# Kernel tuning notes

Hardware: AMD Instinct MI355X
Metric: run time of the kernel (lower is better)

## Reference

```python
import jax, jax.numpy as jnp
import numpy as np

B, H, W, D, C, K, ITERS = 16, 64, 64, 64, 16, 5, 4
EPS_LN = 1e-5

def _ln(x, g, b):
    m = x.mean(-1, keepdims=True)
    v = jnp.mean((x - m) ** 2, axis=-1, keepdims=True)
    return (x - m) / jnp.sqrt(v + EPS_LN) * g + b

def _build_grid(h, w):
    # (h, w, 2) with x in [-1,1] over width, y in [-1,1] over height
    y, x = jnp.meshgrid(jnp.linspace(-1.0, 1.0, h), jnp.linspace(-1.0, 1.0, w), indexing='ij')
    return jnp.stack([x, y], axis=-1)

def _forward(feat, feat_color, mask, slot_noise, slots_mu, slots_logsigma,
             w_grid, b_grid, w_k, w_v, ln_kv_g, ln_kv_b, w_mlp, b_mlp,
             ln_q_g, ln_q_b, w_q, w_ih, w_hh, b_ih, b_hh,
             ln_feat_g, ln_feat_b, ln_color_g, ln_color_b,
             ln_res_g, ln_res_b, w_res, b_res):
    b, h, w, d = feat.shape
    n = h * w
    k_slots = mask.shape[0]
    scale = d ** (-0.5)

    grid = _build_grid(h, w)  # (H, W, 2)

    # fg position: weighted mean of grid under mask -> (K, 2), broadcast to (B, K, 2)
    gm = grid.transpose(2, 0, 1)[None] * mask            # (K, 2, H, W)
    fg_pos = gm.sum((2, 3)) / (mask.sum((2, 3)) + 1e-5)  # (K, 2)
    fg_pos = jnp.broadcast_to(fg_pos[None], (b, k_slots, 2))

    feat_n = _ln(feat.reshape(b, n, d), ln_feat_g, ln_feat_b)                    # (B, N, D)
    featc_n = _ln(feat_color.reshape(b, n, feat_color.shape[-1]), ln_color_g, ln_color_b)

    slot = slots_mu + jnp.exp(slots_logsigma) * slot_noise  # (B, K, D)

    # k/v with relative positional grid embedding (fg_pos is constant across iters,
    # so k/v are iteration-invariant and computed once -- same math as the original loop)
    rel = grid[None, None] - fg_pos[:, :, None, None, :]        # (B, K, H, W, 2)
    rel4 = jnp.concatenate([rel, -rel], -1).reshape(b, k_slots, n, 4)
    grid_embed = rel4 @ w_grid.T + b_grid                       # (B, K, N, D)
    k = _ln(feat_n @ w_k.T[None] [0][None][0][None][0] if False else (feat_n @ w_k.T)[:, None] + grid_embed, ln_kv_g, ln_kv_b) @ w_mlp.T + b_mlp
    v = _ln((feat_n @ w_v.T)[:, None] + grid_embed, ln_kv_g, ln_kv_b) @ w_mlp.T + b_mlp

    attn = None
    for it in range(ITERS):
        prev = slot
        q = _ln(slot, ln_q_g, ln_q_b) @ w_q.T                         # (B, K, D)
        logits = jnp.einsum('bkd,bknd->bkn', q, k) * scale
        attn = jax.nn.softmax(logits, axis=-1)                        # (B, K, N)
        upd = jnp.einsum('bkn,bknd->bkd', attn, v)                    # (B, K, D)
        if it != ITERS - 1:
            # torch GRUCell
            x = upd.reshape(-1, d)
            hp = slot.reshape(-1, d)
            gi = x @ w_ih.T + b_ih
            gh = hp @ w_hh.T + b_hh
            i_r, i_z, i_n = jnp.split(gi, 3, axis=-1)
            h_r, h_z, h_n = jnp.split(gh, 3, axis=-1)
            r = jax.nn.sigmoid(i_r + h_r)
            z = jax.nn.sigmoid(i_z + h_z)
            nn_ = jnp.tanh(i_n + r * h_n)
            slot = ((1.0 - z) * nn_ + z * hp).reshape(b, k_slots, d)
            slot = _ln(slot, ln_res_g, ln_res_b) @ w_res.T + b_res + prev
        else:
            slot_color = jnp.einsum('bkn,bnc->bkc', attn, featc_n)
            slot = jnp.concatenate([slot, slot_color], axis=-1)       # (B, K, D+C)

    amin = attn.min(axis=2, keepdims=True)
    amax = attn.max(axis=2, keepdims=True)
    attn = (attn - amin) / (amax - amin + 1e-5)
    return slot, fg_pos, attn

def setup_inputs() -> dict:
    key = jax.random.key(0)
    ks = jax.random.split(key, 16)
    def rn(i, shape, s=0.02):
        return jax.random.normal(ks[i], shape, jnp.float32) * s
    return {
        'feat': jax.random.normal(ks[0], (B, H, W, D), jnp.float32),
        'feat_color': jax.random.normal(ks[1], (B, H, W, C), jnp.float32),
        'mask': jax.random.uniform(ks[2], (K, 1, H, W), jnp.float32),
        'slot_noise': jax.random.normal(ks[3], (B, K, D), jnp.float32),
        'slots_mu': rn(4, (1, 1, D), 1.0),
        'slots_logsigma': rn(5, (1, 1, D), 0.01),
        'w_grid': rn(6, (D, 4)), 'b_grid': jnp.zeros((D,), jnp.float32),
        'w_k': rn(7, (D, D)), 'w_v': rn(8, (D, D)),
        'ln_kv_g': jnp.ones((D,), jnp.float32), 'ln_kv_b': jnp.zeros((D,), jnp.float32),
        'w_mlp': rn(9, (D, D)), 'b_mlp': jnp.zeros((D,), jnp.float32),
        'ln_q_g': jnp.ones((D,), jnp.float32), 'ln_q_b': jnp.zeros((D,), jnp.float32),
        'w_q': rn(10, (D, D)),
        'w_ih': rn(11, (3 * D, D)), 'w_hh': rn(12, (3 * D, D)),
        'b_ih': jnp.zeros((3 * D,), jnp.float32), 'b_hh': jnp.zeros((3 * D,), jnp.float32),
        'ln_feat_g': jnp.ones((D,), jnp.float32), 'ln_feat_b': jnp.zeros((D,), jnp.float32),
        'ln_color_g': jnp.ones((C,), jnp.float32), 'ln_color_b': jnp.zeros((C,), jnp.float32),
        'ln_res_g': jnp.ones((D,), jnp.float32), 'ln_res_b': jnp.zeros((D,), jnp.float32),
        'w_res': rn(13, (D, D)), 'b_res': jnp.zeros((D,), jnp.float32),
    }

def reference(feat, feat_color, mask, slot_noise, slots_mu, slots_logsigma,
              w_grid, b_grid, w_k, w_v, ln_kv_g, ln_kv_b, w_mlp, b_mlp,
              ln_q_g, ln_q_b, w_q, w_ih, w_hh, b_ih, b_hh,
              ln_feat_g, ln_feat_b, ln_color_g, ln_color_b,
              ln_res_g, ln_res_b, w_res, b_res):
    return _forward(feat, feat_color, mask, slot_noise, slots_mu, slots_logsigma,
                    w_grid, b_grid, w_k, w_v, ln_kv_g, ln_kv_b, w_mlp, b_mlp,
                    ln_q_g, ln_q_b, w_q, w_ih, w_hh, b_ih, b_hh,
                    ln_feat_g, ln_feat_b, ln_color_g, ln_color_b,
                    ln_res_g, ln_res_b, w_res, b_res)
```

## Files before the change

### kernel.cpp

```cpp
#include <hip/hip_runtime.h>
#include <stdint.h>

#define B_ 16
#define H_ 64
#define W_ 64
#define D_ 64
#define C_ 16
#define K_ 5
#define N_ 4096
#define NC_ 32
#define CS_ 128
#define EPS 1e-5f

typedef __attribute__((ext_vector_type(8))) short bf16x8;
typedef __attribute__((ext_vector_type(4))) float f32x4;

__device__ __forceinline__ float wsum64(float v){
  #pragma unroll
  for(int o=1;o<64;o<<=1) v += __shfl_xor(v,o,64);
  return v;
}
__device__ __forceinline__ float wmax64(float v){
  #pragma unroll
  for(int o=1;o<64;o<<=1) v = fmaxf(v, __shfl_xor(v,o,64));
  return v;
}
__device__ __forceinline__ float wmin64(float v){
  #pragma unroll
  for(int o=1;o<64;o<<=1) v = fminf(v, __shfl_xor(v,o,64));
  return v;
}
__device__ __forceinline__ uint16_t f2bf(float f){
  uint32_t u = __float_as_uint(f);
  u += 0x7fffu + ((u>>16)&1u);
  return (uint16_t)(u>>16);
}

__global__ __launch_bounds__(256) void k_pre(
    const float* __restrict__ mask, const float* __restrict__ noise,
    const float* __restrict__ mu, const float* __restrict__ lsg,
    const float* __restrict__ wm, const float* __restrict__ bm, const float* __restrict__ lnkb,
    const float* __restrict__ wk, const float* __restrict__ wv, const float* __restrict__ lnfb,
    const float* __restrict__ wq, const float* __restrict__ lnqg, const float* __restrict__ lnqb,
    const float* __restrict__ wres, const float* __restrict__ bres,
    const float* __restrict__ lnrg, const float* __restrict__ lnrb,
    const float* __restrict__ wih, const float* __restrict__ whh,
    const float* __restrict__ wg, const float* __restrict__ bg,
    const float* __restrict__ lnfg, const float* __restrict__ lnkg,
    float* __restrict__ ws_fg, float* __restrict__ out_fg,
    float* __restrict__ bm2, float* __restrict__ fkb, float* __restrict__ fvb,
    float* __restrict__ qb, float* __restrict__ br2,
    float* __restrict__ wgx, float* __restrict__ wgy, float* __restrict__ gscal,
    float* __restrict__ wrpT,
    float* __restrict__ gw, float* __restrict__ slot, float* __restrict__ out_slot,
    float* __restrict__ WQp, float* __restrict__ WCp, float* __restrict__ bq2p,
    float* __restrict__ uvp, float* __restrict__ vqp, float* __restrict__ cscp){
  __shared__ __align__(16) float M0[64][68];
  __shared__ __align__(16) float M1[64][68];
  __shared__ __align__(16) float M2T[64][68];
  __shared__ float vtmp[4][64];
  __shared__ float aux[4][64];
  int bid=blockIdx.x, tid=threadIdx.x;

  #define MM44(SRCA, SRCB) { \
    float a4[4], b4[4]; \
    *(float4*)a4 = *(const float4*)(SRCA); \
    *(float4*)b4 = *(const float4*)(SRCB); \
    _Pragma("unroll") \
    for(int ii=0;ii<4;ii++){ \
      _Pragma("unroll") \
      for(int jj=0;jj<4;jj++) acc[ii][jj]=fmaf(a4[ii],b4[jj],acc[ii][jj]); \
    } }

  if(bid<5){
    int k=bid;
    float sm=0.f, sx=0.f, sy=0.f;
    for(int p=tid; p<H_*W_; p+=256){
      int i=p>>6, j=p&63;
      float m = mask[k*H_*W_ + p];
      float x = -1.f + (2.f/63.f)*j;
      float y = -1.f + (2.f/63.f)*i;
      sm+=m; sx+=m*x; sy+=m*y;
    }
    __shared__ float r0[4], r1[4], r2[4];
    int wid=tid>>6, lane=tid&63;
    sm=wsum64(sm); sx=wsum64(sx); sy=wsum64(sy);
    if(lane==0){ r0[wid]=sm; r1[wid]=sx; r2[wid]=sy; }
    __syncthreads();
    if(tid==0){
      float tm=r0[0]+r0[1]+r0[2]+r0[3];
      float tx=r1[0]+r1[1]+r1[2]+r1[3];
      float ty=r2[0]+r2[1]+r2[2]+r2[3];
      float px = tx/(tm+1e-5f), py = ty/(tm+1e-5f);
      ws_fg[k*2+0]=px; ws_fg[k*2+1]=py;
      for(int b=0;b<B_;b++){ out_fg[(b*K_+k)*2+0]=px; out_fg[(b*K_+k)*2+1]=py; }
    }
  } else if(bid==5){
    int sel=tid>>6, o=tid&63; float s=0.f;
    if(sel==0){ s=bm[o]; for(int d=0;d<64;d++) s+=lnkb[d]*wm[o*64+d]; bm2[o]=s; }
    else if(sel==1){ for(int d=0;d<64;d++) s+=lnqb[d]*wq[o*64+d]; qb[o]=0.125f*s; }
    else if(sel==2){ for(int d=0;d<64;d++) s+=lnrb[d]*wres[o*64+d]; br2[o]=s+bres[o]; }
    else { for(int d=0;d<64;d++) s+=lnfb[d]*wk[o*64+d]; fkb[o]=s; }
  } else if(bid==6){
    int wv4=tid>>6, l=tid&63;
    if(wv4==0){ float s=0.f; for(int d=0;d<64;d++) s+=lnfb[d]*wv[l*64+d]; fvb[l]=s; }
    else if(wv4==1){
      float4 w4 = *(const float4*)(wg + l*4);
      wgx[l]=w4.x-w4.z; wgy[l]=w4.y-w4.w;
    } else if(wv4==2){
      float4 w4 = *(const float4*)(wg + l*4);
      float wx=w4.x-w4.z, wy=w4.y-w4.w, bl=bg[l];
      float t;
      t=wsum64(wx);    if(l==0) gscal[0]=t*(1.f/64.f);
      t=wsum64(wy);    if(l==0) gscal[1]=t*(1.f/64.f);
      t=wsum64(bl);    if(l==0) gscal[2]=t*(1.f/64.f);
      t=wsum64(wx*wx); if(l==0) gscal[3]=t*(1.f/64.f);
      t=wsum64(wy*wy); if(l==0) gscal[4]=t*(1.f/64.f);
      t=wsum64(wx*wy); if(l==0) gscal[5]=t*(2.f/64.f);
      t=wsum64(wx*bl); if(l==0) gscal[6]=t*(2.f/64.f);
      t=wsum64(wy*bl); if(l==0) gscal[7]=t*(2.f/64.f);
      t=wsum64(bl*bl); if(l==0) gscal[8]=t*(1.f/64.f);
    } else {
      for(int j=l;j<B_*K_*16;j+=64){ int bk2=j>>4, cc2=j&15; out_slot[bk2*80+64+cc2]=0.f; }
    }
  } else if(bid<23){
    int i=(bid-7)*256+tid;
    int d=i>>6, o=i&63;
    wrpT[i]=lnrg[d]*wres[o*64+d];
  } else if(bid<119){
    int i=(bid-23)*256+tid;
    int g6=i>>12, r=i&4095, d=r>>6, o=r&63;
    float v = (g6<3)? wih[(g6*64+o)*64+d] : whh[((g6-3)*64+o)*64+d];
    gw[g6*4096 + d*64 + o] = v;
  } else if(bid<139){
    int i=(bid-119)*256+tid;
    if(i<B_*K_*D_){ int d=i&63; slot[i]=mu[d]+expf(lsg[d])*noise[i]; }
  } else if(bid==139){
    for(int i=tid;i<4096;i+=256){ int r=i>>6,c2=i&63; M0[r][c2]=wq[i]; M1[r][c2]=wm[i]; }
    if(tid>=192){ int l=tid-192;
      float4 w4 = *(const float4*)(wg + l*4);
      aux[0][l]=w4.x-w4.z; aux[1][l]=w4.y-w4.w; aux[2][l]=bg[l]; aux[3][l]=lnkg[l];
    }
    __syncthreads();
    if(tid<64){ float s=0.f; for(int d=0;d<64;d++) s+=lnqb[d]*M0[tid][d]; vtmp[0][tid]=0.125f*s; }
    else if(tid<128){ int c2=tid-64; float s=bm[c2]; for(int d=0;d<64;d++) s+=lnkb[d]*M1[c2][d]; vtmp[1][c2]=s; }
    else if(tid<192){ int o=tid-128; float s=0.f; for(int d=0;d<64;d++) s+=lnfb[d]*wk[o*64+d]; vtmp[2][o]=s; }
    __syncthreads();
    {
      int d0=(tid>>4)*4, e0=(tid&15)*4;
      float acc[4][4]={};
      for(int c2=0;c2<64;c2++) MM44(&M0[c2][d0], &M1[c2][e0]);
      float lq4[4]; *(float4*)lq4 = *(const float4*)(lnqg+d0);
      #pragma unroll
      for(int jj=0;jj<4;jj++){
        float w4[4];
        #pragma unroll
        for(int ii=0;ii<4;ii++) w4[ii]=0.125f*lq4[ii]*acc[ii][jj];
        *(float4*)&M2T[e0+jj][d0] = *(float4*)w4;
      }
    }
    __syncthreads();
    if(tid<64){
      int e=tid; float s=0.f; for(int c2=0;c2<64;c2++) s=fmaf(vtmp[0][c2], M1[c2][e], s); vtmp[3][e]=s;
    } else if(tid<128){
      int d=tid-64; float s=0.f; for(int c2=0;c2<64;c2++) s=fmaf(M0[c2][d], vtmp[1][c2], s);
      vqp[4*64+d]=0.125f*lnqg[d]*s;
    }
    __syncthreads();
    for(int i=tid;i<4096;i+=256){ int e=i>>6,o=i&63; M0[e][o]=aux[3][e]*wk[i]; }
    __syncthreads();
    {
      int d0=(tid>>4)*4, o0=(tid&15)*4;
      float acc[4][4]={};
      for(int e=0;e<64;e++) MM44(&M2T[e][d0], &M0[e][o0]);
      float lf4[4]; *(float4*)lf4 = *(const float4*)(lnfg+o0);
      #pragma unroll
      for(int ii=0;ii<4;ii++){
        float w4[4];
        #pragma unroll
        for(int jj=0;jj<4;jj++) w4[jj]=lf4[jj]*acc[ii][jj];
        *(float4*)(WQp + (d0+ii)*64 + o0) = *(float4*)w4;
      }
    }
    if(tid<64){ int o=tid; float s=0.f;
      for(int e=0;e<64;e++) s=fmaf(vtmp[3][e], M0[e][o], s);
      bq2p[o]=lnfg[o]*s; }
    else if(tid<128){ int d=tid-64; float s1=0.f,sx=0.f,sy=0.f,s3=0.f;
      for(int e=0;e<64;e++){ float pe=M2T[e][d]*aux[3][e];
        s1+=pe; sx+=pe*aux[0][e]; sy+=pe*aux[1][e]; s3+=pe*(aux[2][e]+vtmp[2][e]); }
      vqp[0*64+d]=s1; vqp[1*64+d]=sx; vqp[2*64+d]=sy; vqp[3*64+d]=s3; }
    else if(tid<192){
      int e=tid-128;
      float qe=vtmp[3][e]*aux[3][e];
      float c0=wsum64(qe);
      float c1=wsum64(qe*aux[0][e]);
      float c2=wsum64(qe*aux[1][e]);
      float c3=wsum64(qe*(aux[2][e]+vtmp[2][e]));
      float c4=wsum64(vtmp[0][e]*vtmp[1][e]);
      if(e==0){ cscp[0]=c0; cscp[1]=c1; cscp[2]=c2; cscp[3]=c3; cscp[4]=c4; }
    }
  } else {
    for(int i=tid;i<4096;i+=256){ int r=i>>6,c2=i&63; M0[r][c2]=wv[i]*lnkg[r]; M1[c2][r]=wm[i]; }
    if(tid>=192){ int l=tid-192;
      float4 w4 = *(const float4*)(wg + l*4);
      aux[0][l]=w4.x-w4.z; aux[1][l]=w4.y-w4.w; aux[2][l]=bg[l]; aux[3][l]=lnkg[l];
    }
    __syncthreads();
    if(tid<64){ float s=0.f; const float* wr=wv+tid*64;
      for(int d=0;d<64;d++) s+=lnfb[d]*wr[d]; vtmp[0][tid]=s; }
    __syncthreads();
    {
      int d0=(tid>>4)*4, o0=(tid&15)*4;
      float acc[4][4]={};
      for(int e=0;e<64;e++) MM44(&M0[e][d0], &M1[e][o0]);
      float lf4[4]; *(float4*)lf4 = *(const float4*)(lnfg+d0);
      #pragma unroll
      for(int ii=0;ii<4;ii++){
        float w4[4];
        #pragma unroll
        for(int jj=0;jj<4;jj++) w4[jj]=lf4[ii]*acc[ii][jj];
        *(float4*)(WCp + (d0+ii)*64 + o0) = *(float4*)w4;
      }
    }
    if(tid<64){ int o=tid; float s1=0.f,s2=0.f,s3=0.f,s4=0.f;
      for(int e=0;e<64;e++){ float we=aux[3][e]*M1[e][o];
        s1+=we*(vtmp[0][e]+aux[2][e]); s2+=we*aux[0][e]; s3+=we*aux[1][e]; s4+=we; }
      uvp[0*64+o]=s1; uvp[1*64+o]=s2; uvp[2*64+o]=s3; uvp[3*64+o]=s4; }
  }
  #undef MM44
}

__global__ __launch_bounds__(256) void k_featln(const float* __restrict__ feat,
    const float* __restrict__ wk, const float* __restrict__ wv, const float* __restrict__ gf,
    const float* __restrict__ fkb, const float* __restrict__ fvb,
    const float* __restrict__ wgx, const float* __restrict__ wgy, const float* __restrict__ bg,
    const float* __restrict__ fc, const float* __restrict__ gc, const float* __restrict__ bc,
    uint16_t* __restrict__ Aout, float4* __restrict__ kstat, float4* __restrict__ vstat,
    float* __restrict__ fcn){
  int tid=threadIdx.x, wid=tid>>6, lane=tid&63;
  int q=lane>>4, c=lane&15;
  size_t row = (size_t)blockIdx.x*64 + wid*16 + c;
  const float* xp = feat + row*64;
  float x[16];
  *(float4*)&x[0]  = *(const float4*)(xp + q*8);
  *(float4*)&x[4]  = *(const float4*)(xp + q*8 + 4);
  *(float4*)&x[8]  = *(const float4*)(xp + 32 + q*8);
  *(float4*)&x[12] = *(const float4*)(xp + 36 + q*8);
  float s=0.f;
  #pragma unroll
  for(int i=0;i<16;i++) s+=x[i];
  s += __shfl_xor(s,16,64); s += __shfl_xor(s,32,64);
  float mean = s*(1.f/64.f);
  float v=0.f;
  #pragma unroll
  for(int i=0;i<16;i++){ float d=x[i]-mean; v+=d*d; }
  v += __shfl_xor(v,16,64); v += __shfl_xor(v,32,64);
  float rs = rsqrtf(v*(1.f/64.f)+EPS);
  float gl[16];
  *(float4*)&gl[0]  = *(const float4*)(gf + q*8);
  *(float4*)&gl[4]  = *(const float4*)(gf + q*8 + 4);
  *(float4*)&gl[8]  = *(const float4*)(gf + 32 + q*8);
  *(float4*)&gl[12] = *(const float4*)(gf + 36 + q*8);
  bf16x8 A0, A1;
  #pragma unroll
  for(int j=0;j<8;j++){
    A0[j] = (short)f2bf((x[j]  -mean)*rs);
    A1[j] = (short)f2bf((x[8+j]-mean)*rs);
  }
  *(bf16x8*)(Aout + row*64 + q*8) = A0;
  *(bf16x8*)(Aout + row*64 + 32 + q*8) = A1;
  float wgxl[4][4], wgyl[4][4], bgl[4][4];
  #pragma unroll
  for(int ot=0;ot<4;ot++){
    *(float4*)&wgxl[ot][0] = *(const float4*)(wgx + ot*16 + q*4);
    *(float4*)&wgyl[ot][0] = *(const float4*)(wgy + ot*16 + q*4);
    *(float4*)&bgl[ot][0]  = *(const float4*)(bg + ot*16 + q*4);
  }
  #pragma unroll
  for(int mat=0;mat<2;mat++){
    const float* w = mat? wv : wk;
    const float* fb = mat? fvb : fkb;
    float ss=0.f, s2=0.f, dx=0.f, dy=0.f, db=0.f;
    #pragma unroll
    for(int ot=0; ot<4; ot++){
      const float* wp = w + (size_t)(ot*16+c)*64 + q*8;
      bf16x8 W0, W1;
      #pragma unroll
      for(int j=0;j<8;j++){ W0[j]=(short)f2bf(wp[j]*gl[j]); W1[j]=(short)f2bf(wp[32+j]*gl[8+j]); }
      float4 bq = *(const float4*)(fb + ot*16 + q*4);
      f32x4 acc = {bq.x,bq.y,bq.z,bq.w};
      acc = __builtin_amdgcn_mfma_f32_16x16x32_bf16(W0, A0, acc, 0,0,0);
      acc = __builtin_amdgcn_mfma_f32_16x16x32_bf16(W1, A1, acc, 0,0,0);
      #pragma unroll
      for(int r=0;r<4;r++){
        float a=acc[r];
        ss+=a; s2+=a*a;
        dx = fmaf(a, wgxl[ot][r], dx);
        dy = fmaf(a, wgyl[ot][r], dy);
        db = fmaf(a, bgl[ot][r], db);
      }
    }
    ss += __shfl_xor(ss,16,64); ss += __shfl_xor(ss,32,64);
    s2 += __shfl_xor(s2,16,64); s2 += __shfl_xor(s2,32,64);
    dx += __shfl_xor(dx,16,64); dx += __shfl_xor(dx,32,64);
    dy += __shfl_xor(dy,16,64); dy += __shfl_xor(dy,32,64);
    db += __shfl_xor(db,16,64); db += __shfl_xor(db,32,64);
    if(lane<16){
      size_t row2 = (size_t)blockIdx.x*64 + wid*16 + lane;
      float4 st = { ss*(1.f/64.f), s2*(1.f/64.f)+db*(1.f/32.f), dx*(1.f/32.f), dy*(1.f/32.f) };
      (mat? vstat : kstat)[row2] = st;
    }
  }
  int r16=tid>>4, cc=tid&15;
  #pragma unroll
  for(int i=0;i<4;i++){
    size_t row2 = (size_t)blockIdx.x*64 + i*16 + r16;
    float xv = fc[row2*16+cc];
    float sc=xv;
    #pragma unroll
    for(int o=1;o<16;o<<=1) sc += __shfl_xor(sc,o,16);
    float m2 = sc*(1.f/16.f);
    float df = xv-m2;
    float v2 = df*df;
    #pragma unroll
    for(int o=1;o<16;o<<=1) v2 += __shfl_xor(v2,o,16);
    fcn[row2*16+cc] = df*rsqrtf(v2*(1.f/16.f)+EPS)*gc[cc] + bc[cc];
  }
}

template<bool GRU>
__global__ __launch_bounds__(256) void k_slotq(
    const float* __restrict__ slot_prev, float* __restrict__ slot_cur,
    const float* __restrict__ part, const float* __restrict__ pscal,
    const float* __restrict__ red_in,
    const float* __restrict__ gw,
    const float* __restrict__ bih, const float* __restrict__ bhh,
    const float* __restrict__ wrpT, const float* __restrict__ br2,
    const float* __restrict__ bm2,
    const float* __restrict__ WQ, const float* __restrict__ bq2,
    const float* __restrict__ WC, const float* __restrict__ uvec,
    const float* __restrict__ vq, const float* __restrict__ csc,
    const float* __restrict__ gscal,
    float* __restrict__ qs_out, float* __restrict__ cst_out){
  __shared__ float vv[64], vh[64];
  __shared__ float red6[4][64][6];
  __shared__ float lamb[NC_];
  __shared__ float sc4[4];
  int bk=blockIdx.x;
  int tid=threadIdx.x, wid=tid>>6, lane=tid&63;
  int o=lane, qq=wid;
  float mwgx=gscal[0], mwgy=gscal[1], mbg=gscal[2];

  #define MV(Wptr) { float p_=0.f; \
      _Pragma("unroll") \
      for(int dd=0;dd<16;dd++) p_ = fmaf(vv[qq*16+dd], (Wptr)[(qq*16+dd)*64+o], p_); \
      red6[qq][o][0]=p_; } __syncthreads();
  #define SUM0 (red6[0][lane][0]+red6[1][lane][0]+red6[2][lane][0]+red6[3][lane][0])

  float cur=0.f, hp=0.f;
  if(GRU){
    if(wid==0){
      float m_l = (lane<NC_)? red_in[((size_t)bk*NC_+lane)*4]   : -1e30f;
      float s_l = (lane<NC_)? red_in[((size_t)bk*NC_+lane)*4+1] : 0.f;
      float M = wmax64(m_l);
      float eu = (lane<NC_)? __expf(m_l-M) : 0.f;
      float S = wsum64(s_l*eu);
      float lam = eu/S;
      if(lane<NC_) lamb[lane]=lam;
      float p0 = (lane<NC_)? pscal[((size_t)bk*NC_+lane)*4+0] : 0.f;
      float p1 = (lane<NC_)? pscal[((size_t)bk*NC_+lane)*4+1] : 0.f;
      float p2 = (lane<NC_)? pscal[((size_t)bk*NC_+lane)*4+2] : 0.f;
      float p3 = (lane<NC_)? pscal[((size_t)bk*NC_+lane)*4+3] : 0.f;
      float As = wsum64(lam*p0), Ax = wsum64(lam*p1);
      float Ay = wsum64(lam*p2), Am = wsum64(lam*p3);
      if(lane==0){ sc4[0]=As; sc4[1]=Ax; sc4[2]=Ay; sc4[3]=Am; }
    }
    __syncthreads();
    {
      float p_=0.f;
      #pragma unroll
      for(int j=0;j<8;j++){
        int cc = qq*8+j;
        p_ = fmaf(lamb[cc], part[((size_t)bk*NC_+cc)*64+o], p_);
      }
      red6[qq][o][0]=p_;
    }
    __syncthreads();
    if(wid==0) vv[lane] = SUM0;
    __syncthreads();
    MV(WC);
    if(wid==0){
      float As=sc4[0],Ax=sc4[1],Ay=sc4[2],Am=sc4[3];
      float x_ = SUM0 + As*uvec[lane] + Ax*uvec[64+lane] + Ay*uvec[128+lane]
               - Am*uvec[192+lane] + bm2[lane];
      hp = slot_prev[bk*64+lane];
      vv[lane]=x_; vh[lane]=hp;
    }
    __syncthreads();
    {
      float p0=0.f,p1=0.f,p2=0.f,p3=0.f,p4=0.f,p5=0.f;
      #pragma unroll
      for(int dd=0;dd<16;dd++){
        int d = qq*16+dd;
        float xd=vv[d], hd=vh[d];
        p0 = fmaf(xd, gw[d*64+o], p0);
        p1 = fmaf(xd, gw[4096+d*64+o], p1);
        p2 = fmaf(xd, gw[8192+d*64+o], p2);
        p3 = fmaf(hd, gw[12288+d*64+o], p3);
        p4 = fmaf(hd, gw[16384+d*64+o], p4);
        p5 = fmaf(hd, gw[20480+d*64+o], p5);
      }
      red6[qq][o][0]=p0; red6[qq][o][1]=p1; red6[qq][o][2]=p2;
      red6[qq][o][3]=p3; red6[qq][o][4]=p4; red6[qq][o][5]=p5;
    }
    __syncthreads();
    if(wid==0){
      float gir=bih[lane], giz=bih[64+lane], gin=bih[128+lane];
      float ghr=bhh[lane], ghz=bhh[64+lane], ghn=bhh[128+lane];
      #pragma unroll
      for(int w=0;w<4;w++){
        gir+=red6[w][lane][0]; giz+=red6[w][lane][1]; gin+=red6[w][lane][2];
        ghr+=red6[w][lane][3]; ghz+=red6[w][lane][4]; ghn+=red6[w][lane][5];
      }
      float r=1.f/(1.f+__expf(-(gir+ghr)));
      float z=1.f/(1.f+__expf(-(giz+ghz)));
      float nn=tanhf(gin+r*ghn);
      float sp=(1.f-z)*nn+z*hp;
      float m=wsum64(sp)*(1.f/64.f); float df=sp-m;
      float var=wsum64(df*df)*(1.f/64.f);
      vv[lane]=df*rsqrtf(var+EPS);
    }
    __syncthreads();
    MV(wrpT);
    if(wid==0){
      cur = SUM0 + br2[lane] + hp;
      slot_cur[bk*64+lane]=cur;
    }
  } else {
    if(wid==0) cur = slot_prev[bk*64+lane];
  }
  __syncthreads();
  if(wid==0){
    float m=wsum64(cur)*(1.f/64.f); float df=cur-m;
    float var=wsum64(df*df)*(1.f/64.f);
    float LNc=df*rsqrtf(var+EPS);
    vv[lane]=LNc;
    float s1=wsum64(LNc*vq[lane])     + csc[0];
    float c1=wsum64(LNc*vq[64+lane])  + csc[1];
    float c2=wsum64(LNc*vq[128+lane]) + csc[2];
    float c3=wsum64(LNc*vq[192+lane]) + csc[3];
    float c4=wsum64(LNc*vq[256+lane]) + csc[4];
    if(lane==0){
      float* cp = cst_out + bk*8;
      cp[0]=c1-s1*mwgx; cp[1]=c2-s1*mwgy; cp[2]=c3-s1*mbg; cp[3]=s1; cp[4]=c4;
    }
  }
  __syncthreads();
  MV(WQ);
  if(wid==0) qs_out[bk*64+lane] = SUM0 + bq2[lane];
  #undef MV
  #undef SUM0
}

template<bool FINAL>
__global__ __launch_bounds__(256) void k_attn(const uint16_t* __restrict__ Aw,
    const float4* __restrict__ kstat, const float4* __restrict__ vstat,
    const float* __restrict__ qsg, const float* __restrict__ cstg,
    const float* __restrict__ gscal, const float* __restrict__ ws_fg,
    float* __restrict__ lgt, float* __restrict__ red_out,
    float* __restrict__ part_o, float* __restrict__ pscal_o){
  __shared__ uint32_t As_[CS_*32];
  __shared__ __align__(16) float dps[5][CS_+4];
  __shared__ float pw[4][5][64];
  __shared__ float rm[2][5], rn[2][5];
  __shared__ float rsc[2][5][5];
  __shared__ float cstl[5][5];
  __shared__ float fgl[5][2];
  int chunk=blockIdx.x, b=blockIdx.y;
  int tid=threadIdx.x, wid=tid>>6, lane=tid&63;
  int c=lane&15, q=lane>>4;
  float mwgx=gscal[0], mwgy=gscal[1], mbg=gscal[2];
  float g1=gscal[3], g2=gscal[4], g3=gscal[5], g4=gscal[6], g5=gscal[7], g6=gscal[8];

  if(!FINAL){
    const uint4* Ag = (const uint4*)(Aw + ((size_t)b*N_ + chunk*CS_)*64);
    #pragma unroll
    for(int jj=0;jj<4;jj++){
      int f = jj*256 + tid;
      *(uint4*)(As_ + f*4) = Ag[f];
    }
  }
  if(tid<25) cstl[tid/5][tid%5] = cstg[(b*K_ + tid/5)*8 + (tid%5)];
  if(tid>=32 && tid<42){ int i2=tid-32; fgl[i2>>1][i2&1] = ws_fg[i2]; }
  int half = wid & 1;
  int r128 = half*64 + lane;
  int nrow = chunk*CS_ + r128;
  int k0 = (wid < 2) ? 0 : 3;
  int nk = (wid < 2) ? 3 : 2;
  float4 st = kstat[(size_t)b*N_ + nrow];
  float4 sv;
  if(!FINAL) sv = vstat[(size_t)b*N_ + nrow];
  float gx = -1.f + (2.f/63.f)*(nrow&63);
  float gy = -1.f + (2.f/63.f)*(nrow>>6);
  __syncthreads();

  {
    bf16x8 QF0={0,0,0,0,0,0,0,0}, QF1={0,0,0,0,0,0,0,0};
    if(c<5){
      const float* qpp = qsg + (b*K_+c)*64;
      #pragma unroll
      for(int j=0;j<8;j++){
        QF0[j] = (short)f2bf(qpp[q*8+j]);
        QF1[j] = (short)f2bf(qpp[32+q*8+j]);
      }
    }
    const uint16_t* Abase = Aw + ((size_t)b*N_ + chunk*CS_)*64;
    #pragma unroll
    for(int it=0;it<2;it++){
      int tile = wid*32 + it*16;
      const uint16_t* rp = Abase + (size_t)(tile+c)*64;
      bf16x8 BF0 = *(const bf16x8*)(rp + q*8);
      bf16x8 BF1 = *(const bf16x8*)(rp + 32 + q*8);
      f32x4 acc = {0.f,0.f,0.f,0.f};
      acc = __builtin_amdgcn_mfma_f32_16x16x32_bf16(QF0, BF0, acc, 0,0,0);
      acc = __builtin_amdgcn_mfma_f32_16x16x32_bf16(QF1, BF1, acc, 0,0,0);
      #pragma unroll
      for(int r=0;r<4;r++){
        int s = q*4+r;
        if(s<5) dps[s][tile+c]=acc[r];
      }
    }
  }
  __syncthreads();

  float l3[3], w3[3];
  #pragma unroll
  for(int j=0;j<3;j++){
    if(j<nk){
      int k=k0+j;
      float rx = gx - fgl[k][0], ry = gy - fgl[k][1];
      float CX=cstl[k][0], CY=cstl[k][1], C0=cstl[k][2], S1=cstl[k][3], C4=cstl[k][4];
      float quad = g1*rx*rx + g2*ry*ry + g3*rx*ry + g4*rx + g5*ry + g6;
      float mu = st.x + rx*mwgx + ry*mwgy + mbg;
      float var = st.y + rx*st.z + ry*st.w + quad - mu*mu;
      float rsn = rsqrtf(var+EPS);
      float l = rsn*(dps[k][r128] + rx*CX + ry*CY + C0 - S1*st.x) + C4;
      l3[j]=l;
      float wmx = wmax64(l);
      if(lane==0) rm[half][k]=wmx;
      if(FINAL){ float mn=wmin64(l); if(lane==0) rn[half][k]=mn; }
    }
  }
  __syncthreads();
  #pragma unroll
  for(int j=0;j<3;j++){
    if(j<nk){
      int k=k0+j;
      float m_c = fmaxf(rm[0][k], rm[1][k]);
      float e = __expf(l3[j]-m_c);
      float scq = wsum64(e);
      if(!FINAL){
        float rx = gx - fgl[k][0], ry = gy - fgl[k][1];
        float quad = g1*rx*rx + g2*ry*ry + g3*rx*ry + g4*rx + g5*ry + g6;
        float muV = sv.x + rx*mwgx + ry*mwgy + mbg;
        float varV = sv.y + rx*sv.z + ry*sv.w + quad - muV*muV;
        float rsv_ = rsqrtf(varV+EPS);
        float w_ = e*rsv_;
        w3[j]=w_;
        float As2=wsum64(w_), Ax2=wsum64(w_*rx), Ay2=wsum64(w_*ry), Am2=wsum64(w_*muV);
        if(lane==0){ rsc[half][k][0]=scq; rsc[half][k][1]=As2; rsc[half][k][2]=Ax2;
                     rsc[half][k][3]=Ay2; rsc[half][k][4]=Am2; }
      } else {
        lgt[(size_t)(b*K_+k)*N_ + nrow] = l3[j];
        if(lane==0) rsc[half][k][0]=scq;
      }
    }
  }
  __syncthreads();
  if(tid<5){
    int k=tid;
    size_t idx = ((size_t)(b*K_+k)*NC_+chunk)*4;
    red_out[idx+0]=fmaxf(rm[0][k],rm[1][k]);
    red_out[idx+1]=rsc[0][k][0]+rsc[1][k][0];
    if(FINAL) red_out[idx+2]=fminf(rn[0][k],rn[1][k]);
    if(!FINAL){
      pscal_o[idx+0]=rsc[0][k][1]+rsc[1][k][1];
      pscal_o[idx+1]=rsc[0][k][2]+rsc[1][k][2];
      pscal_o[idx+2]=rsc[0][k][3]+rsc[1][k][3];
      pscal_o[idx+3]=rsc[0][k][4]+rsc[1][k][4];
    }
  }
  if(!FINAL){
    #pragma unroll
    for(int j=0;j<3;j++)
      if(j<nk) dps[k0+j][r128]=w3[j];
  }

  if(!FINAL){
    __syncthreads();
    const uint16_t* Au = (const uint16_t*)As_;
    float a0=0.f,a1=0.f,a2=0.f,a3=0.f,a4=0.f;
    #pragma unroll
    for(int rb=0;rb<8;rb++){
      int row0 = wid*32 + rb*4;
      float4 d0 = *(const float4*)&dps[0][row0];
      float4 d1 = *(const float4*)&dps[1][row0];
      float4 d2 = *(const float4*)&dps[2][row0];
      float4 d3 = *(const float4*)&dps[3][row0];
      float4 d4 = *(const float4*)&dps[4][row0];
      float av0 = __uint_as_float(((uint32_t)Au[(row0+0)*64+lane])<<16);
      float av1 = __uint_as_float(((uint32_t)Au[(row0+1)*64+lane])<<16);
      float av2 = __uint_as_float(((uint32_t)Au[(row0+2)*64+lane])<<16);
      float av3 = __uint_as_float(((uint32_t)Au[(row0+3)*64+lane])<<16);
      a0=fmaf(d0.x,av0,a0); a0=fmaf(d0.y,av1,a0); a0=fmaf(d0.z,av2,a0); a0=fmaf(d0.w,av3,a0);
      a1=fmaf(d1.x,av0,a1); a1=fmaf(d1.y,av1,a1); a1=fmaf(d1.z,av2,a1); a1=fmaf(d1.w,av3,a1);
      a2=fmaf(d2.x,av0,a2); a2=fmaf(d2.y,av1,a2); a2=fmaf(d2.z,av2,a2); a2=fmaf(d2.w,av3,a2);
      a3=fmaf(d3.x,av0,a3); a3=fmaf(d3.y,av1,a3); a3=fmaf(d3.z,av2,a3); a3=fmaf(d3.w,av3,a3);
      a4=fmaf(d4.x,av0,a4); a4=fmaf(d4.y,av1,a4); a4=fmaf(d4.z,av2,a4); a4=fmaf(d4.w,av3,a4);
    }
    pw[wid][0][lane]=a0; pw[wid][1][lane]=a1; pw[wid][2][lane]=a2;
    pw[wid][3][lane]=a3; pw[wid][4][lane]=a4;
    __syncthreads();
    if(tid<64){
      #pragma unroll
      for(int k=0;k<5;k++){
        float s2 = pw[0][k][tid]+pw[1][k][tid]+pw[2][k][tid]+pw[3][k][tid];
        part_o[((size_t)(b*K_+k)*NC_+chunk)*64 + tid] = s2;
      }
    }
  }
}

__global__ __launch_bounds__(256) void k_fin(const float* __restrict__ lgt,
    const float* __restrict__ red, const float* __restrict__ featc,
    const float* __restrict__ sl1, float* __restrict__ out_slot,
    float* __restrict__ out_attn){
  __shared__ float psp[CS_];
  __shared__ float pcz[4][16];
  int chunk=blockIdx.x, bk=blockIdx.y, b=bk/K_;
  int tid=threadIdx.x, wid=tid>>6, lane=tid&63, sub=lane>>4, c4=lane&15;
  const float* rp = red + (size_t)bk*NC_*4;
  float M=-1e30f;
  #pragma unroll
  for(int i=0;i<NC_;i++) M = fmaxf(M, rp[i*4]);
  float S=0.f;
  #pragma unroll
  for(int i=0;i<NC_;i++) S += rp[i*4+1]*__expf(rp[i*4]-M);
  float invS = 1.f/S;
  float LMIN=1e30f;
  #pragma unroll
  for(int i=0;i<NC_;i++) LMIN=fminf(LMIN, rp[i*4+2]);
  float amin = __expf(LMIN-M)*invS;
  float dinv = 1.f/(invS - amin + 1e-5f);
  const float* lp = lgt + (size_t)bk*N_ + chunk*CS_;
  if(tid<CS_){
    float p = __expf(lp[tid]-M)*invS;
    psp[tid]=p;
    out_attn[(size_t)bk*N_ + chunk*CS_ + tid] = (p - amin)*dinv;
  }
  __syncthreads();
  const float* Fb = featc + ((size_t)b*N_ + chunk*CS_)*16;
  float ac=0.f;
  for(int t=0;t<8;t++){
    int n = wid*32 + t*4 + sub;
    ac += psp[n]*Fb[(size_t)n*16 + c4];
  }
  ac+=__shfl_xor(ac,16,64); ac+=__shfl_xor(ac,32,64);
  if(lane<16) pcz[wid][lane]=ac;
  __syncthreads();
  if(tid<16){
    float s2 = pcz[0][tid]+pcz[1][tid]+pcz[2][tid]+pcz[3][tid];
    atomicAdd(&out_slot[bk*80+64+tid], s2);
  }
  if(chunk==0 && tid<64) out_slot[bk*80+tid]=sl1[bk*64+tid];
}

extern "C" void kernel_launch(void* const* d_in, const int* in_sizes, int n_in,
                              void* d_out, int out_size, void* d_ws, size_t ws_size,
                              hipStream_t stream){
  (void)in_sizes; (void)n_in; (void)out_size; (void)ws_size;
  const float* feat = (const float*)d_in[0];
  const float* featc= (const float*)d_in[1];
  const float* mask = (const float*)d_in[2];
  const float* noise= (const float*)d_in[3];
  const float* mu   = (const float*)d_in[4];
  const float* lsg  = (const float*)d_in[5];
  const float* wg   = (const float*)d_in[6];
  const float* bg   = (const float*)d_in[7];
  const float* wk   = (const float*)d_in[8];
  const float* wv   = (const float*)d_in[9];
  const float* lnkg = (const float*)d_in[10];
  const float* lnkb = (const float*)d_in[11];
  const float* wm   = (const float*)d_in[12];
  const float* bm   = (const float*)d_in[13];
  const float* lnqg = (const float*)d_in[14];
  const float* lnqb = (const float*)d_in[15];
  const float* wq   = (const float*)d_in[16];
  const float* wih  = (const float*)d_in[17];
  const float* whh  = (const float*)d_in[18];
  const float* bih  = (const float*)d_in[19];
  const float* bhh  = (const float*)d_in[20];
  const float* lnfg = (const float*)d_in[21];
  const float* lnfb = (const float*)d_in[22];
  const float* lncg = (const float*)d_in[23];
  const float* lncb = (const float*)d_in[24];
  const float* lnrg = (const float*)d_in[25];
  const float* lnrb = (const float*)d_in[26];
  const float* wres = (const float*)d_in[27];
  const float* bres = (const float*)d_in[28];

  float* out = (float*)d_out;
  float* out_slot = out;
  float* out_fg   = out + 6400;
  float* out_attn = out + 6560;

  float* wsf     = (float*)d_ws;
  float* ws_fg   = wsf;
  float* ws_bm2  = wsf + 16;
  float* ws_fkb  = ws_bm2 + 64;
  float* ws_fvb  = ws_fkb + 64;
  float* ws_qb   = ws_fvb + 64;
  float* ws_br2  = ws_qb + 64;
  float* ws_wgx  = ws_br2 + 64;
  float* ws_wgy  = ws_wgx + 64;
  float* ws_gs   = ws_wgy + 64;
  float* ws_wrpT = ws_gs + 16;
  float* ws_gw   = ws_wrpT + 4096;
  float* ws_WQ   = ws_gw + 24576;
  float* ws_WC   = ws_WQ + 4096;
  float* ws_bq2  = ws_WC + 4096;
  float* ws_u    = ws_bq2 + 64;
  float* ws_vq   = ws_u + 256;
  float* ws_csc  = ws_vq + 320;
  float* ws_qs   = ws_csc + 16;
  float* ws_cst  = ws_qs + B_*K_*D_;
  float* ws_fc   = ws_cst + 640;
  float* ws_sl0  = ws_fc + (size_t)B_*N_*C_;
  float* ws_sl1  = ws_sl0 + B_*K_*D_;
  float* ws_lgt  = ws_sl1 + B_*K_*D_;
  float* ws_red0 = ws_lgt + (size_t)B_*K_*N_;
  float* ws_red1 = ws_red0 + B_*K_*NC_*4;
  float* ws_prt0 = ws_red1 + B_*K_*NC_*4;
  float* ws_prt1 = ws_prt0 + (size_t)B_*K_*NC_*64;
  float* ws_psc0 = ws_prt1 + (size_t)B_*K_*NC_*64;
  float* ws_psc1 = ws_psc0 + B_*K_*NC_*4;
  float4* ws_kst = (float4*)(ws_psc1 + B_*K_*NC_*4);
  float4* ws_vst = ws_kst + (size_t)B_*N_;
  uint16_t* ws_A = (uint16_t*)(ws_vst + (size_t)B_*N_);

  k_pre<<<141,256,0,stream>>>(mask,noise,mu,lsg, wm,bm,lnkb, wk,wv,lnfb,
                              wq,lnqg,lnqb, wres,bres,lnrg,lnrb, wih,whh, wg,bg,
                              lnfg,lnkg,
                              ws_fg,out_fg, ws_bm2,ws_fkb,ws_fvb,ws_qb,ws_br2,
                              ws_wgx,ws_wgy,ws_gs,
                              ws_wrpT, ws_gw, ws_sl0, out_slot,
                              ws_WQ, ws_WC, ws_bq2, ws_u, ws_vq, ws_csc);
  k_featln<<<(B_*N_)/64,256,0,stream>>>(feat,wk,wv,lnfg,ws_fkb,ws_fvb,
                                        ws_wgx,ws_wgy,bg,
                                        featc,lncg,lncb,
                                        ws_A,ws_kst,ws_vst,ws_fc);

  dim3 agrid(NC_,B_);
  #define SQ_ARGS(SPREV,SCUR,PIN,SCIN,RIN) SPREV,SCUR,PIN,SCIN,RIN,ws_gw, \
      bih,bhh,ws_wrpT,ws_br2,ws_bm2, ws_WQ,ws_bq2, ws_WC,ws_u, ws_vq,ws_csc, \
      ws_gs, ws_qs,ws_cst
  #define AT_ARGS(ROUT,POUT,SCOUT) ws_A,ws_kst,ws_vst,ws_qs,ws_cst,ws_gs,ws_fg, \
      ws_lgt,ROUT,POUT,SCOUT

  k_slotq<false><<<B_*K_,256,0,stream>>>(SQ_ARGS(ws_sl0,ws_sl0,ws_prt1,ws_psc1,ws_red1));
  k_attn<false><<<agrid,256,0,stream>>>(AT_ARGS(ws_red0,ws_prt0,ws_psc0));
  k_slotq<true><<<B_*K_,256,0,stream>>>(SQ_ARGS(ws_sl0,ws_sl1,ws_prt0,ws_psc0,ws_red0));
  k_attn<false><<<agrid,256,0,stream>>>(AT_ARGS(ws_red1,ws_prt1,ws_psc1));
  k_slotq<true><<<B_*K_,256,0,stream>>>(SQ_ARGS(ws_sl1,ws_sl0,ws_prt1,ws_psc1,ws_red1));
  k_attn<false><<<agrid,256,0,stream>>>(AT_ARGS(ws_red0,ws_prt0,ws_psc0));
  k_slotq<true><<<B_*K_,256,0,stream>>>(SQ_ARGS(ws_sl0,ws_sl1,ws_prt0,ws_psc0,ws_red0));
  k_attn<true><<<agrid,256,0,stream>>>(AT_ARGS(ws_red1,ws_prt1,ws_psc1));
  k_fin<<<dim3(NC_,B_*K_),256,0,stream>>>(ws_lgt,ws_red1,ws_fc,ws_sl1,out_slot,out_attn);
}
```

Measured before the change: 221.3 us.

## Halve attention chunk size to 64 rows, one wave per slot

Chunk size drops from 128 to 64 rows, so there are 64 chunks per batch and twice as many attention and finalize blocks. Each wave now owns one slot over all 64 rows, so the softmax max is computed inside the wave and the cross-half shared-memory reduction and one barrier go away. The GRU kernel's chunk reduction and the finalize kernel are updated for 64 chunks, and the finalize kernel reads its per-chunk stats as float4 in a fused loop. In exchange there are more partial results to reduce, and wave 0 carries an extra slot, which unbalances the waves.

Result: slower. 226.4 us (+2.3%).

```diff
diff --git a/kernel.cpp b/kernel.cpp
--- a/kernel.cpp
+++ b/kernel.cpp
@@ -8,8 +8,8 @@
 #define C_ 16
 #define K_ 5
 #define N_ 4096
-#define NC_ 32
-#define CS_ 128
+#define NC_ 64
+#define CS_ 64
 #define EPS 1e-5f
 
 typedef __attribute__((ext_vector_type(8))) short bf16x8;
@@ -360,17 +360,17 @@
   float cur=0.f, hp=0.f;
   if(GRU){
     if(wid==0){
-      float m_l = (lane<NC_)? red_in[((size_t)bk*NC_+lane)*4]   : -1e30f;
-      float s_l = (lane<NC_)? red_in[((size_t)bk*NC_+lane)*4+1] : 0.f;
+      float m_l = red_in[((size_t)bk*NC_+lane)*4];
+      float s_l = red_in[((size_t)bk*NC_+lane)*4+1];
       float M = wmax64(m_l);
-      float eu = (lane<NC_)? __expf(m_l-M) : 0.f;
+      float eu = __expf(m_l-M);
       float S = wsum64(s_l*eu);
       float lam = eu/S;
-      if(lane<NC_) lamb[lane]=lam;
-      float p0 = (lane<NC_)? pscal[((size_t)bk*NC_+lane)*4+0] : 0.f;
-      float p1 = (lane<NC_)? pscal[((size_t)bk*NC_+lane)*4+1] : 0.f;
-      float p2 = (lane<NC_)? pscal[((size_t)bk*NC_+lane)*4+2] : 0.f;
-      float p3 = (lane<NC_)? pscal[((size_t)bk*NC_+lane)*4+3] : 0.f;
+      lamb[lane]=lam;
+      float p0 = pscal[((size_t)bk*NC_+lane)*4+0];
+      float p1 = pscal[((size_t)bk*NC_+lane)*4+1];
+      float p2 = pscal[((size_t)bk*NC_+lane)*4+2];
+      float p3 = pscal[((size_t)bk*NC_+lane)*4+3];
       float As = wsum64(lam*p0), Ax = wsum64(lam*p1);
       float Ay = wsum64(lam*p2), Am = wsum64(lam*p3);
       if(lane==0){ sc4[0]=As; sc4[1]=Ax; sc4[2]=Ay; sc4[3]=Am; }
@@ -379,8 +379,8 @@
     {
       float p_=0.f;
       #pragma unroll
-      for(int j=0;j<8;j++){
-        int cc = qq*8+j;
+      for(int j=0;j<16;j++){
+        int cc = qq*16+j;
         p_ = fmaf(lamb[cc], part[((size_t)bk*NC_+cc)*64+o], p_);
       }
       red6[qq][o][0]=p_;
@@ -472,8 +472,8 @@
   __shared__ uint32_t As_[CS_*32];
   __shared__ __align__(16) float dps[5][CS_+4];
   __shared__ float pw[4][5][64];
-  __shared__ float rm[2][5], rn[2][5];
-  __shared__ float rsc[2][5][5];
+  __shared__ float rm[5], rn[5];
+  __shared__ float rsc[5][5];
   __shared__ float cstl[5][5];
   __shared__ float fgl[5][2];
   int chunk=blockIdx.x, b=blockIdx.y;
@@ -485,18 +485,14 @@
   if(!FINAL){
     const uint4* Ag = (const uint4*)(Aw + ((size_t)b*N_ + chunk*CS_)*64);
     #pragma unroll
-    for(int jj=0;jj<4;jj++){
+    for(int jj=0;jj<2;jj++){
       int f = jj*256 + tid;
       *(uint4*)(As_ + f*4) = Ag[f];
     }
   }
   if(tid<25) cstl[tid/5][tid%5] = cstg[(b*K_ + tid/5)*8 + (tid%5)];
   if(tid>=32 && tid<42){ int i2=tid-32; fgl[i2>>1][i2&1] = ws_fg[i2]; }
-  int half = wid & 1;
-  int r128 = half*64 + lane;
-  int nrow = chunk*CS_ + r128;
-  int k0 = (wid < 2) ? 0 : 3;
-  int nk = (wid < 2) ? 3 : 2;
+  int nrow = chunk*CS_ + lane;
   float4 st = kstat[(size_t)b*N_ + nrow];
   float4 sv;
   if(!FINAL) sv = vstat[(size_t)b*N_ + nrow];
@@ -515,64 +511,49 @@
       }
     }
     const uint16_t* Abase = Aw + ((size_t)b*N_ + chunk*CS_)*64;
+    int tile = wid*16;
+    const uint16_t* rp = Abase + (size_t)(tile+c)*64;
+    bf16x8 BF0 = *(const bf16x8*)(rp + q*8);
+    bf16x8 BF1 = *(const bf16x8*)(rp + 32 + q*8);
+    f32x4 acc = {0.f,0.f,0.f,0.f};
+    acc = __builtin_amdgcn_mfma_f32_16x16x32_bf16(QF0, BF0, acc, 0,0,0);
+    acc = __builtin_amdgcn_mfma_f32_16x16x32_bf16(QF1, BF1, acc, 0,0,0);
     #pragma unroll
-    for(int it=0;it<2;it++){
-      int tile = wid*32 + it*16;
-      const uint16_t* rp = Abase + (size_t)(tile+c)*64;
-      bf16x8 BF0 = *(const bf16x8*)(rp + q*8);
-      bf16x8 BF1 = *(const bf16x8*)(rp + 32 + q*8);
-      f32x4 acc = {0.f,0.f,0.f,0.f};
-      acc = __builtin_amdgcn_mfma_f32_16x16x32_bf16(QF0, BF0, acc, 0,0,0);
-      acc = __builtin_amdgcn_mfma_f32_16x16x32_bf16(QF1, BF1, acc, 0,0,0);
-      #pragma unroll
-      for(int r=0;r<4;r++){
-        int s = q*4+r;
-        if(s<5) dps[s][tile+c]=acc[r];
-      }
+    for(int r=0;r<4;r++){
+      int s = q*4+r;
+      if(s<5) dps[s][tile+c]=acc[r];
     }
   }
   __syncthreads();
 
-  float l3[3], w3[3];
-  #pragma unroll
-  for(int j=0;j<3;j++){
-    if(j<nk){
-      int k=k0+j;
+  int nsl = (wid==0)? 2 : 1;
+  #pragma unroll
+  for(int j=0;j<2;j++){
+    if(j<nsl){
+      int k = (j==0)? wid : 4;
       float rx = gx - fgl[k][0], ry = gy - fgl[k][1];
       float CX=cstl[k][0], CY=cstl[k][1], C0=cstl[k][2], S1=cstl[k][3], C4=cstl[k][4];
       float quad = g1*rx*rx + g2*ry*ry + g3*rx*ry + g4*rx + g5*ry + g6;
       float mu = st.x + rx*mwgx + ry*mwgy + mbg;
       float var = st.y + rx*st.z + ry*st.w + quad - mu*mu;
       float rsn = rsqrtf(var+EPS);
-      float l = rsn*(dps[k][r128] + rx*CX + ry*CY + C0 - S1*st.x) + C4;
-      l3[j]=l;
-      float wmx = wmax64(l);
-      if(lane==0) rm[half][k]=wmx;
-      if(FINAL){ float mn=wmin64(l); if(lane==0) rn[half][k]=mn; }
-    }
-  }
-  __syncthreads();
-  #pragma unroll
-  for(int j=0;j<3;j++){
-    if(j<nk){
-      int k=k0+j;
-      float m_c = fmaxf(rm[0][k], rm[1][k]);
-      float e = __expf(l3[j]-m_c);
+      float l = rsn*(dps[k][lane] + rx*CX + ry*CY + C0 - S1*st.x) + C4;
+      float m_c = wmax64(l);
+      float e = __expf(l-m_c);
       float scq = wsum64(e);
       if(!FINAL){
-        float rx = gx - fgl[k][0], ry = gy - fgl[k][1];
-        float quad = g1*rx*rx + g2*ry*ry + g3*rx*ry + g4*rx + g5*ry + g6;
         float muV = sv.x + rx*mwgx + ry*mwgy + mbg;
         float varV = sv.y + rx*sv.z + ry*sv.w + quad - muV*muV;
         float rsv_ = rsqrtf(varV+EPS);
         float w_ = e*rsv_;
-        w3[j]=w_;
         float As2=wsum64(w_), Ax2=wsum64(w_*rx), Ay2=wsum64(w_*ry), Am2=wsum64(w_*muV);
-        if(lane==0){ rsc[half][k][0]=scq; rsc[half][k][1]=As2; rsc[half][k][2]=Ax2;
-                     rsc[half][k][3]=Ay2; rsc[half][k][4]=Am2; }
+        if(lane==0){ rm[k]=m_c; rsc[k][0]=scq; rsc[k][1]=As2; rsc[k][2]=Ax2;
+                     rsc[k][3]=Ay2; rsc[k][4]=Am2; }
+        dps[k][lane] = w_;
       } else {
-        lgt[(size_t)(b*K_+k)*N_ + nrow] = l3[j];
-        if(lane==0) rsc[half][k][0]=scq;
+        float mn = wmin64(l);
+        lgt[(size_t)(b*K_+k)*N_ + nrow] = l;
+        if(lane==0){ rm[k]=m_c; rn[k]=mn; rsc[k][0]=scq; }
       }
     }
   }
@@ -580,29 +561,23 @@
   if(tid<5){
     int k=tid;
     size_t idx = ((size_t)(b*K_+k)*NC_+chunk)*4;
-    red_out[idx+0]=fmaxf(rm[0][k],rm[1][k]);
-    red_out[idx+1]=rsc[0][k][0]+rsc[1][k][0];
-    if(FINAL) red_out[idx+2]=fminf(rn[0][k],rn[1][k]);
+    red_out[idx+0]=rm[k];
+    red_out[idx+1]=rsc[k][0];
+    if(FINAL) red_out[idx+2]=rn[k];
     if(!FINAL){
-      pscal_o[idx+0]=rsc[0][k][1]+rsc[1][k][1];
-      pscal_o[idx+1]=rsc[0][k][2]+rsc[1][k][2];
-      pscal_o[idx+2]=rsc[0][k][3]+rsc[1][k][3];
-      pscal_o[idx+3]=rsc[0][k][4]+rsc[1][k][4];
-    }
-  }
+      pscal_o[idx+0]=rsc[k][1];
+      pscal_o[idx+1]=rsc[k][2];
+      pscal_o[idx+2]=rsc[k][3];
+      pscal_o[idx+3]=rsc[k][4];
+    }
+  }
+
   if(!FINAL){
-    #pragma unroll
-    for(int j=0;j<3;j++)
-      if(j<nk) dps[k0+j][r128]=w3[j];
-  }
-
-  if(!FINAL){
-    __syncthreads();
     const uint16_t* Au = (const uint16_t*)As_;
     float a0=0.f,a1=0.f,a2=0.f,a3=0.f,a4=0.f;
     #pragma unroll
-    for(int rb=0;rb<8;rb++){
-      int row0 = wid*32 + rb*4;
+    for(int rb=0;rb<4;rb++){
+      int row0 = wid*16 + rb*4;
       float4 d0 = *(const float4*)&dps[0][row0];
       float4 d1 = *(const float4*)&dps[1][row0];
       float4 d2 = *(const float4*)&dps[2][row0];
@@ -639,17 +614,14 @@
   __shared__ float pcz[4][16];
   int chunk=blockIdx.x, bk=blockIdx.y, b=bk/K_;
   int tid=threadIdx.x, wid=tid>>6, lane=tid&63, sub=lane>>4, c4=lane&15;
-  const float* rp = red + (size_t)bk*NC_*4;
+  const float4* rp4 = (const float4*)(red + (size_t)bk*NC_*4);
   float M=-1e30f;
   #pragma unroll
-  for(int i=0;i<NC_;i++) M = fmaxf(M, rp[i*4]);
-  float S=0.f;
-  #pragma unroll
-  for(int i=0;i<NC_;i++) S += rp[i*4+1]*__expf(rp[i*4]-M);
+  for(int i=0;i<NC_;i++) M = fmaxf(M, rp4[i].x);
+  float S=0.f, LMIN=1e30f;
+  #pragma unroll
+  for(int i=0;i<NC_;i++){ float4 r4=rp4[i]; S += r4.y*__expf(r4.x-M); LMIN=fminf(LMIN, r4.z); }
   float invS = 1.f/S;
-  float LMIN=1e30f;
-  #pragma unroll
-  for(int i=0;i<NC_;i++) LMIN=fminf(LMIN, rp[i*4+2]);
   float amin = __expf(LMIN-M)*invS;
   float dinv = 1.f/(invS - amin + 1e-5f);
   const float* lp = lgt + (size_t)bk*N_ + chunk*CS_;
@@ -661,8 +633,9 @@
   __syncthreads();
   const float* Fb = featc + ((size_t)b*N_ + chunk*CS_)*16;
   float ac=0.f;
-  for(int t=0;t<8;t++){
-    int n = wid*32 + t*4 + sub;
+  #pragma unroll
+  for(int t=0;t<4;t++){
+    int n = wid*16 + t*4 + sub;
     ac += psp[n]*Fb[(size_t)n*16 + c4];
   }
   ac+=__shfl_xor(ac,16,64); ac+=__shfl_xor(ac,32,64);
```
